# Optimization experiments

Hardware: AMD Instinct MI355X
Metric: run time of the kernel (lower is better)

Reference implementation:

```python
import jax, jax.numpy as jnp
import numpy as np

B, N, C, H = 16, 1024, 768, 12
GRID = 32  # 32x32 patch grid -> N = 1024 tokens
ROPE_BASE = 10000.0


def setup_inputs() -> dict:
    key = jax.random.key(0)
    k1, k2, k3 = jax.random.split(key, 3)
    x = jax.random.normal(k1, (B, N, C), dtype=jnp.float32)
    W_qkv = jax.random.normal(k2, (C, 3 * C), dtype=jnp.float32) * 0.02
    b_qkv = jnp.zeros((3 * C,), dtype=jnp.float32)
    W_proj = jax.random.normal(k3, (C, C), dtype=jnp.float32) * 0.02
    b_proj = jnp.zeros((C,), dtype=jnp.float32)
    ids = jnp.arange(N)
    pos_h = jnp.broadcast_to(ids // GRID, (B, N)).astype(jnp.int32)
    pos_w = jnp.broadcast_to(ids % GRID, (B, N)).astype(jnp.int32)
    return dict(x=x, W_qkv=W_qkv, b_qkv=b_qkv, W_proj=W_proj, b_proj=b_proj,
                pos_h=pos_h, pos_w=pos_w, num_heads=H)


def _rotate_half(t):
    t1, t2 = jnp.split(t, 2, axis=-1)
    return jnp.concatenate((-t2, t1), axis=-1)


def _rope_1d(t, pos, inv):
    # t: (B,H,N,d_rope), pos: (B,N), inv: (d_rope//2,)
    p = pos.astype(jnp.float32)[..., None] * inv      # (B,N,d_rope//2)
    p = p[:, None]                                    # (B,1,N,d_rope//2)
    cos = jnp.repeat(jnp.cos(p), 2, axis=-1)          # repeat_interleave(2)
    sin = jnp.repeat(jnp.sin(p), 2, axis=-1)
    return t * cos + _rotate_half(t) * sin


def reference(x, W_qkv, b_qkv, W_proj, b_proj, pos_h, pos_w, num_heads):
    Bx, Nx, Cx = x.shape
    hd = Cx // num_heads
    d_rope = hd // 2
    inv = 1.0 / ROPE_BASE ** (jnp.arange(0, d_rope, 2, dtype=jnp.float32) / float(max(d_rope, 1)))
    qkv = (x @ W_qkv + b_qkv).reshape(Bx, Nx, 3, num_heads, hd).transpose(2, 0, 3, 1, 4)
    q, k, v = qkv[0], qkv[1], qkv[2]                  # each (B,H,N,hd)
    # 2D RoPE: row-half / col-half of head_dim
    qh, qw = jnp.split(q, 2, axis=-1)
    kh, kw = jnp.split(k, 2, axis=-1)
    qh = _rope_1d(qh, pos_h, inv); kh = _rope_1d(kh, pos_h, inv)
    qw = _rope_1d(qw, pos_w, inv); kw = _rope_1d(kw, pos_w, inv)
    q = jnp.concatenate((qh, qw), axis=-1)
    k = jnp.concatenate((kh, kw), axis=-1)
    scale = hd ** -0.5
    attn = jax.nn.softmax(jnp.einsum('bhnd,bhmd->bhnm', q, k) * scale, axis=-1)
    out = jnp.einsum('bhnm,bhmd->bhnd', attn, v).transpose(0, 2, 1, 3).reshape(Bx, Nx, Cx)
    return out @ W_proj + b_proj
```

## Files before the change

kernel.cpp:

```cpp
#include <hip/hip_runtime.h>
#include <hip/hip_bf16.h>

#define B_ 16
#define N_ 1024
#define C_ 768
#define H_ 12
#define HD_ 64
#define QC_ (3*C_)

using bf16 = __hip_bfloat16;
using bf16x8 = __attribute__((ext_vector_type(8))) __bf16;
using f32x4  = __attribute__((ext_vector_type(4))) float;

__device__ __forceinline__ float tof(bf16 v){ return __bfloat162float(v); }

__device__ __forceinline__ void gload16(const void* g, void* l) {
  __builtin_amdgcn_global_load_lds(
      (const __attribute__((address_space(1))) unsigned int*)g,
      (__attribute__((address_space(3))) unsigned int*)l, 16, 0, 0);
}

__device__ __forceinline__ int xcd_swizzle(int bid, int nwg) {
  return (bid & 7) * (nwg >> 3) + (bid >> 3);
}

__device__ __forceinline__ unsigned pk2(float a, float b) {
  unsigned ua = (unsigned)__bfloat16_as_ushort(__float2bfloat16(a));
  unsigned ub = (unsigned)__bfloat16_as_ushort(__float2bfloat16(b));
  return ua | (ub << 16);
}

__global__ __launch_bounds__(256) void detect_dtype(
    const unsigned* __restrict__ x32, int* __restrict__ flag)
{
  __shared__ int cnt;
  if (threadIdx.x == 0) cnt = 0;
  __syncthreads();
  int local = 0;
  #pragma unroll
  for (int i = 0; i < 16; i++) {
    unsigned u = x32[threadIdx.x * 16 + i * 4096];
    unsigned e = (u >> 7) & 0xFF;
    local += (e >= 110 && e <= 140) ? 1 : 0;
  }
  atomicAdd(&cnt, local);
  __syncthreads();
  if (threadIdx.x == 0) *flag = (cnt > 2048) ? 1 : 0;
}

__global__ __launch_bounds__(256) void cvt_x(
    const void* __restrict__ x, bf16* __restrict__ xb,
    const int* __restrict__ flag, const int n4, const int off4)
{
  const int i = blockIdx.x * 256 + threadIdx.x;
  if (i >= n4) return;
  if (*flag) {
    ((uint2*)xb)[i] = ((const uint2*)x)[off4 + i];
  } else {
    float4 v = ((const float4*)x)[off4 + i];
    xb[i*4+0] = __float2bfloat16(v.x);
    xb[i*4+1] = __float2bfloat16(v.y);
    xb[i*4+2] = __float2bfloat16(v.z);
    xb[i*4+3] = __float2bfloat16(v.w);
  }
}

__global__ __launch_bounds__(256) void wt_cvt(
    const void* __restrict__ W, bf16* __restrict__ WT,
    const int K, const int Nd, const int* __restrict__ flag)
{
  __shared__ float t[32][33];
  const int fl = *flag;
  const int n0 = blockIdx.x * 32, k0 = blockIdx.y * 32;
  const int tx = threadIdx.x & 31, ty = threadIdx.x >> 5;
  for (int kk = ty; kk < 32; kk += 8) {
    const size_t gi = (size_t)(k0 + kk) * Nd + (n0 + tx);
    t[kk][tx] = fl ? tof(((const bf16*)W)[gi]) : ((const float*)W)[gi];
  }
  __syncthreads();
  for (int nn = ty; nn < 32; nn += 8)
    WT[(size_t)(n0 + nn) * K + (k0 + tx)] = __float2bfloat16(t[tx][nn]);
}

__global__ __launch_bounds__(256) void gemm_qkv_rope(
    const bf16* __restrict__ Ab, const bf16* __restrict__ WT,
    const void* __restrict__ bias, bf16* __restrict__ Qp,
    bf16* __restrict__ Kp, bf16* __restrict__ Vtb,
    const int* __restrict__ flag,
    const int* __restrict__ pos_h, const int* __restrict__ pos_w)
{
  const int K = C_;
  const bool bbf = (*flag != 0);

  __shared__ __align__(16) char smem[36864];
  unsigned short* As = (unsigned short*)smem;
  unsigned short* Bs = (unsigned short*)(smem + 16384);

  const int tid = threadIdx.x;
  const int l   = tid & 63;
  const int w   = tid >> 6;
  const int wm  = (w & 1) * 64;
  const int wn  = (w >> 1) * 64;

  const int nwg = gridDim.x * gridDim.y;
  const int bid = blockIdx.y * gridDim.x + blockIdx.x;
  const int lb  = xcd_swizzle(bid, nwg);
  const int gy  = gridDim.y;
  const int brow = lb / gy;
  const int bcol = lb - brow * gy;
  const int row0 = brow * 128;
  const int col0 = bcol * 128;

  const int srow = w*8 + (l >> 3);
  const int sch  = (l & 7) ^ (l >> 3);
  const bf16* Ast = Ab + (size_t)(row0 + srow) * K + sch * 8;
  const bf16* Bst = WT + (size_t)(col0 + srow) * K + sch * 8;

  f32x4 acc[4][4] = {};

  for (int k0 = 0; k0 < K; k0 += 64) {
    __syncthreads();
    #pragma unroll
    for (int i = 0; i < 4; i++) {
      gload16(Ast + (size_t)i*32*K + k0, As + (i*32 + w*8)*64);
      gload16(Bst + (size_t)i*32*K + k0, Bs + (i*32 + w*8)*64);
    }
    __syncthreads();
    #pragma unroll
    for (int s = 0; s < 2; s++) {
      bf16x8 af[4], bg[4];
      const int ch = (s*4 + (l >> 4)) ^ (l & 7);
      #pragma unroll
      for (int i = 0; i < 4; i++) {
        const int rowm = wm + i*16 + (l & 15);
        const int rown = wn + i*16 + (l & 15);
        af[i] = *(const bf16x8*)&As[rowm*64 + ch*8];
        bg[i] = *(const bf16x8*)&Bs[rown*64 + ch*8];
      }
      #pragma unroll
      for (int i = 0; i < 4; i++)
        #pragma unroll
        for (int j = 0; j < 4; j++)
          acc[i][j] = __builtin_amdgcn_mfma_f32_16x16x32_bf16(
                          af[i], bg[j], acc[i][j], 0, 0, 0);
    }
  }

  const int colbase = col0 + wn;
  const int t   = colbase / 768;
  const int h   = (colbase % 768) >> 6;
  const int dd0 = l & 15;
  float bv4[4];
  #pragma unroll
  for (int j = 0; j < 4; j++) {
    const int c = colbase + dd0 + j*16;
    bv4[j] = bbf ? tof(((const bf16*)bias)[c]) : ((const float*)bias)[c];
  }
  const int rb = row0 + wm + (l >> 4) * 4;

  __syncthreads();
  bf16* Ts = (bf16*)(smem + w * 9216);

  if (t == 2) {
    #pragma unroll
    for (int i = 0; i < 4; i++) {
      #pragma unroll
      for (int v = 0; v < 4; v++) {
        const int nl = i*16 + ((l >> 4) << 2) + v;
        #pragma unroll
        for (int j = 0; j < 4; j++) {
          const int dl = dd0 + j*16;
          const float y = acc[i][j][v] + bv4[j];
          Ts[dl*72 + (((nl >> 3) ^ (dl & 7)) << 3) + (nl & 7)] =
              __float2bfloat16(y);
        }
      }
    }
  } else {
    const int fi  = dd0 >> 1;
    const float LOG2B = 13.287712379549449f;
    const float f1 = exp2f(-LOG2B * (float)fi       * (1.0f/16.0f));
    const float f2 = exp2f(-LOG2B * (float)(fi + 8) * (1.0f/16.0f));
    #pragma unroll
    for (int i = 0; i < 4; i++) {
      #pragma unroll
      for (int v = 0; v < 4; v++) {
        const int r  = rb + i*16 + v;
        const int rl = i*16 + (l >> 4)*4 + v;
        float y0 = acc[i][0][v] + bv4[0];
        float y1 = acc[i][1][v] + bv4[1];
        float y2 = acc[i][2][v] + bv4[2];
        float y3 = acc[i][3][v] + bv4[3];
        const float ph = (float)pos_h[r];
        const float pw = (float)pos_w[r];
        float s1,c1,s2,c2,s3,c3,s4,c4;
        __sincosf(ph*f1, &s1, &c1);
        __sincosf(ph*f2, &s2, &c2);
        __sincosf(pw*f1, &s3, &c3);
        __sincosf(pw*f2, &s4, &c4);
        float z[4];
        z[0] = y0*c1 - y1*s1;
        z[1] = y1*c2 + y0*s2;
        z[2] = y2*c3 - y3*s3;
        z[3] = y3*c4 + y2*s4;
        if (t == 0) { z[0]*=0.125f; z[1]*=0.125f; z[2]*=0.125f; z[3]*=0.125f; }
        #pragma unroll
        for (int j = 0; j < 4; j++) {
          const int cl = dd0 + j*16;
          Ts[rl*72 + (((cl >> 3) ^ (rl & 7)) << 3) + (cl & 7)] =
              __float2bfloat16(z[j]);
        }
      }
    }
  }
  __syncthreads();

  if (t == 2) {
    const int n0 = (row0 + wm) & 1023;
    const int bp = (row0 + wm) >> 10;
    const size_t gbase = (size_t)(bp*12 + h) * 65536;
    #pragma unroll
    for (int dr = 0; dr < 8; dr++) {
      const int dl = dr*8 + (l >> 3);
      const int c  = l & 7;
      uint4 vv = *(const uint4*)&Ts[dl*72 + ((c ^ (dl & 7)) << 3)];
      *(uint4*)&Vtb[gbase + (size_t)dl*1024 + n0 + c*8] = vv;
    }
  } else {
    bf16* dst = (t == 0) ? Qp : Kp;
    const int rg0 = row0 + wm;
    const int bp  = rg0 >> 10;
    const int nb  = rg0 & 1023;
    const size_t gbase = (size_t)(bp*12 + h) * 65536;
    #pragma unroll
    for (int dr = 0; dr < 8; dr++) {
      const int rl = dr*8 + (l >> 3);
      const int c  = l & 7;
      uint4 vv = *(const uint4*)&Ts[rl*72 + ((c ^ (rl & 7)) << 3)];
      *(uint4*)&dst[gbase + (size_t)(nb + rl)*64 + c*8] = vv;
    }
  }
}

__global__ __launch_bounds__(256) void attn_mfma(
    const bf16* __restrict__ Qp, const bf16* __restrict__ Kp,
    const bf16* __restrict__ Vtb, bf16* __restrict__ ao)
{
  __shared__ __align__(16) bf16 Qs[64*64];
  __shared__ __align__(16) bf16 Ks[64*64];
  __shared__ __align__(16) bf16 Vs[64*64];
  __shared__ __align__(16) bf16 Ps[64*64];
  const int tid = threadIdx.x;
  const int l   = tid & 63;
  const int w   = tid >> 6;

  const int nwg = gridDim.x * gridDim.y;
  const int bid = blockIdx.y * gridDim.x + blockIdx.x;
  const int lb  = xcd_swizzle(bid, nwg);
  const int qt  = lb & 15;
  const int bh  = lb >> 4;
  const size_t base = (size_t)bh * 65536;

  const int srow = w*8 + (l >> 3);
  const int sch  = (l & 7) ^ (l >> 3);
  const bf16* Qst = Qp  + base + (size_t)(qt*64 + srow)*64 + sch*8;
  const bf16* Kst = Kp  + base + (size_t)srow*64   + sch*8;
  const bf16* Vst = Vtb + base + (size_t)srow*1024 + sch*8;

  #pragma unroll
  for (int i = 0; i < 2; i++)
    gload16(Qst + (size_t)i*32*64, Qs + (i*32 + w*8)*64);
  __syncthreads();

  bf16x8 af[2];
  {
    const int row = w*16 + (l & 15);
    #pragma unroll
    for (int s = 0; s < 2; s++) {
      const int ch = (s*4 + (l >> 4)) ^ (row & 7);
      af[s] = *(const bf16x8*)&Qs[row*64 + ch*8];
    }
  }

  const float LOG2E = 1.4426950408889634f;
  float m_i = -3.0e38f, l_i = 0.f;
  f32x4 o[4] = {};

  const int g    = l >> 4;
  const int qrow = w*16 + (l & 15);

  for (int kt = 0; kt < 16; kt++) {
    __syncthreads();
    #pragma unroll
    for (int i = 0; i < 2; i++) {
      gload16(Kst + (size_t)(kt*64 + i*32)*64, Ks + (i*32 + w*8)*64);
      gload16(Vst + (size_t)i*32*1024 + kt*64, Vs + (i*32 + w*8)*64);
    }
    __syncthreads();

    f32x4 s[4];
    #pragma unroll
    for (int nt = 0; nt < 4; nt++) {
      f32x4 a = {};
      const int nrow = nt*16 + (l & 15);
      #pragma unroll
      for (int ss = 0; ss < 2; ss++) {
        const int ch = (ss*4 + (l >> 4)) ^ (nrow & 7);
        bf16x8 bg = *(const bf16x8*)&Ks[nrow*64 + ch*8];
        a = __builtin_amdgcn_mfma_f32_16x16x32_bf16(bg, af[ss], a, 0, 0, 0);
      }
      s[nt] = a;
    }

    float mloc = s[0][0];
    #pragma unroll
    for (int nt = 0; nt < 4; nt++)
      #pragma unroll
      for (int v = 0; v < 4; v++)
        mloc = fmaxf(mloc, s[nt][v]);
    mloc = fmaxf(mloc, __shfl_xor(mloc, 16));
    const float m0 = fmaxf(mloc, __shfl_xor(mloc, 32));

    if (!__all(m0 - m_i <= 8.0f)) {
      const float mx = fmaxf(m_i, m0);
      const float alpha = exp2f((m_i - mx) * LOG2E);
      l_i *= alpha;
      m_i = mx;
      float a_o[4];
      #pragma unroll
      for (int v = 0; v < 4; v++)
        a_o[v] = __shfl(alpha, (l & 48) | ((g << 2) + v));
      #pragma unroll
      for (int nt = 0; nt < 4; nt++)
        #pragma unroll
        for (int v = 0; v < 4; v++)
          o[nt][v] *= a_o[v];
    }

    float r = 0.f;
    #pragma unroll
    for (int nt = 0; nt < 4; nt++)
      #pragma unroll
      for (int v = 0; v < 4; v++) {
        const float p = exp2f((s[nt][v] - m_i) * LOG2E);
        s[nt][v] = p;
        r += p;
      }
    r += __shfl_xor(r, 16);
    r += __shfl_xor(r, 32);
    l_i += r;

    #pragma unroll
    for (int nt = 0; nt < 4; nt++) {
      const int k0 = nt*16 + (g << 2);
      const int ch = (k0 >> 3) ^ (qrow & 7);
      uint2 uu;
      uu.x = pk2(s[nt][0], s[nt][1]);
      uu.y = pk2(s[nt][2], s[nt][3]);
      *(uint2*)&Ps[qrow*64 + ch*8 + (k0 & 7)] = uu;
    }

    #pragma unroll
    for (int ss = 0; ss < 2; ss++) {
      const int prow = w*16 + (l & 15);
      const int pch  = (ss*4 + (l >> 4)) ^ (prow & 7);
      bf16x8 pa = *(const bf16x8*)&Ps[prow*64 + pch*8];
      #pragma unroll
      for (int ntd = 0; ntd < 4; ntd++) {
        const int drow = ntd*16 + (l & 15);
        const int vch  = (ss*4 + (l >> 4)) ^ (drow & 7);
        bf16x8 vb = *(const bf16x8*)&Vs[drow*64 + vch*8];
        o[ntd] = __builtin_amdgcn_mfma_f32_16x16x32_bf16(pa, vb, o[ntd], 0,0,0);
      }
    }
  }

  const int b = bh / 12, h = bh - b*12;
  const float inv = 1.0f / l_i;
  float inv_o[4];
  #pragma unroll
  for (int v = 0; v < 4; v++)
    inv_o[v] = __shfl(inv, (l & 48) | ((g << 2) + v));
  #pragma unroll
  for (int v = 0; v < 4; v++) {
    const int rl = g*4 + v;
    #pragma unroll
    for (int ntd = 0; ntd < 4; ntd++) {
      const int cl = ntd*16 + (l & 15);
      Ps[(w*16 + rl)*64 + (((cl >> 3) ^ (rl & 7)) << 3) + (cl & 7)] =
          __float2bfloat16(o[ntd][v] * inv_o[v]);
    }
  }
  #pragma unroll
  for (int e = 0; e < 2; e++) {
    const int rl = e*8 + (l >> 3);
    const int c  = l & 7;
    uint4 vv = *(const uint4*)&Ps[(w*16 + rl)*64 + ((c ^ (rl & 7)) << 3)];
    const int r = qt*64 + w*16 + rl;
    *(uint4*)&ao[((size_t)(b*1024 + r)) * 768 + h*64 + c*8] = vv;
  }
}

__global__ __launch_bounds__(256) void gemm_mfma(
    const bf16* __restrict__ Ab, const bf16* __restrict__ WT,
    const void* __restrict__ bias, void* __restrict__ Cout,
    const int Nd, const int K, const int c_row_off,
    const int* __restrict__ flag, const int bias_mode, const int c_mode)
{
  const int fl = *flag;
  const bool bbf = (bias_mode == 2) ? (fl != 0) : (bias_mode != 0);
  const bool cbf = (c_mode == 2) ? (fl != 0) : (c_mode != 0);

  __shared__ __align__(16) unsigned short As[128*64];
  __shared__ __align__(16) unsigned short Bs[128*64];

  const int tid = threadIdx.x;
  const int l   = tid & 63;
  const int w   = tid >> 6;
  const int wm  = (w & 1) * 64;
  const int wn  = (w >> 1) * 64;

  const int nwg = gridDim.x * gridDim.y;
  const int bid = blockIdx.y * gridDim.x + blockIdx.x;
  const int lb  = xcd_swizzle(bid, nwg);
  const int gy  = gridDim.y;
  const int brow = lb / gy;
  const int bcol = lb - brow * gy;
  const int row0 = brow * 128;
  const int col0 = bcol * 128;

  const int srow = w*8 + (l >> 3);
  const int sch  = (l & 7) ^ (l >> 3);
  const bf16* Ast = Ab + (size_t)(row0 + srow) * K + sch * 8;
  const bf16* Bst = WT + (size_t)(col0 + srow) * K + sch * 8;

  f32x4 acc[4][4] = {};

  for (int k0 = 0; k0 < K; k0 += 64) {
    __syncthreads();
    #pragma unroll
    for (int i = 0; i < 4; i++) {
      gload16(Ast + (size_t)i*32*K + k0, As + (i*32 + w*8)*64);
      gload16(Bst + (size_t)i*32*K + k0, Bs + (i*32 + w*8)*64);
    }
    __syncthreads();
    #pragma unroll
    for (int s = 0; s < 2; s++) {
      bf16x8 af[4], bg[4];
      const int ch = (s*4 + (l >> 4)) ^ (l & 7);
      #pragma unroll
      for (int i = 0; i < 4; i++) {
        const int rowm = wm + i*16 + (l & 15);
        const int rown = wn + i*16 + (l & 15);
        af[i] = *(const bf16x8*)&As[rowm*64 + ch*8];
        bg[i] = *(const bf16x8*)&Bs[rown*64 + ch*8];
      }
      #pragma unroll
      for (int i = 0; i < 4; i++)
        #pragma unroll
        for (int j = 0; j < 4; j++)
          acc[i][j] = __builtin_amdgcn_mfma_f32_16x16x32_bf16(
                          af[i], bg[j], acc[i][j], 0, 0, 0);
    }
  }

  const int cn    = col0 + wn + (l & 15);
  const int rbase = c_row_off + row0 + wm + (l >> 4) * 4;
  #pragma unroll
  for (int j = 0; j < 4; j++) {
    const int col = cn + j*16;
    const float bval = bbf ? tof(((const bf16*)bias)[col])
                           : ((const float*)bias)[col];
    #pragma unroll
    for (int i = 0; i < 4; i++) {
      #pragma unroll
      for (int v = 0; v < 4; v++) {
        const size_t r = (size_t)(rbase + i*16 + v);
        const float val = acc[i][j][v] + bval;
        if (cbf) ((bf16*)Cout)[r * Nd + col] = __float2bfloat16(val);
        else     ((float*)Cout)[r * Nd + col] = val;
      }
    }
  }
}

extern "C" void kernel_launch(void* const* d_in, const int* in_sizes, int n_in,
                              void* d_out, int out_size, void* d_ws, size_t ws_size,
                              hipStream_t stream)
{
  (void)in_sizes; (void)n_in; (void)out_size;
  const void* x     = d_in[0];
  const void* Wqkv  = d_in[1];
  const void* bqkv  = d_in[2];
  const void* Wproj = d_in[3];
  const void* bproj = d_in[4];
  const int*  pos_h = (const int*)d_in[5];
  const int*  pos_w = (const int*)d_in[6];

  int* flag = (int*)d_ws;
  char* p = (char*)d_ws + 256;
  bf16* WqkvT  = (bf16*)p; p += (size_t)QC_ * C_ * 2;
  bf16* WprojT = (bf16*)p; p += (size_t)C_ * C_ * 2;

  const size_t fixed = 256 + (size_t)QC_*C_*2 + (size_t)C_*C_*2;
  const size_t perb  = 5 * (size_t)N_ * C_ * 2;
  int CB = 16;
  if (ws_size < fixed + 16*perb) CB = 8;
  if (ws_size < fixed + 8*perb)  CB = 4;
  if (ws_size < fixed + 4*perb)  CB = 2;
  if (ws_size < fixed + 2*perb)  CB = 1;
  const int Mc = CB * N_;
  const size_t tsz = (size_t)Mc * C_;

  bf16* xb  = (bf16*)p;
  bf16* Qp  = xb  + tsz;
  bf16* Kp  = Qp  + tsz;
  bf16* Vtb = Kp  + tsz;
  bf16* ao  = Vtb + tsz;

  detect_dtype<<<1, 256, 0, stream>>>((const unsigned*)x, flag);
  wt_cvt<<<dim3(QC_/32, C_/32), 256, 0, stream>>>(Wqkv, WqkvT, C_, QC_, flag);
  wt_cvt<<<dim3(C_/32,  C_/32), 256, 0, stream>>>(Wproj, WprojT, C_, C_, flag);

  for (int c0 = 0; c0 < B_; c0 += CB) {
    const int n4 = Mc * C_ / 4;
    cvt_x<<<(n4 + 255)/256, 256, 0, stream>>>(x, xb, flag, n4, c0 * N_ * C_ / 4);
    gemm_qkv_rope<<<dim3(Mc/128, QC_/128), 256, 0, stream>>>(
        xb, WqkvT, bqkv, Qp, Kp, Vtb, flag,
        pos_h + (size_t)c0*N_, pos_w + (size_t)c0*N_);
    attn_mfma<<<dim3(N_/64, CB*H_), 256, 0, stream>>>(Qp, Kp, Vtb, ao);
    gemm_mfma<<<dim3(Mc/128, C_/128), 256, 0, stream>>>(
        ao, WprojT, bproj, d_out, C_, C_, c0*N_, flag, 2, 2);
  }
}
```

Measured before the change: 368.7 us.

## Fold log2e into Q scale, compute row sums via MFMA, alias Q/P LDS

Folds the log2(e) factor into the Q scaling during the QKV epilogue, so the attention softmax can use exp2 directly without a multiply. The row-sum reduction with shuffles is replaced by an extra MFMA against a vector of ones, accumulating l in the same layout as O. Q and P now share one LDS buffer to cut shared memory per block, and s_setprio hints are placed around the MFMA phases. This trades a little accuracy for fewer VALU ops, since P is rounded to bf16 before being summed, and it relies on Q being read into registers before P overwrites the shared buffer.

```diff
diff --git a/kernel.cpp b/kernel.cpp
--- a/kernel.cpp
+++ b/kernel.cpp
@@ -203,7 +203,10 @@
         z[1] = y1*c2 + y0*s2;
         z[2] = y2*c3 - y3*s3;
         z[3] = y3*c4 + y2*s4;
-        if (t == 0) { z[0]*=0.125f; z[1]*=0.125f; z[2]*=0.125f; z[3]*=0.125f; }
+        if (t == 0) {
+          const float QS = 0.18033688011112042f;
+          z[0]*=QS; z[1]*=QS; z[2]*=QS; z[3]*=QS;
+        }
         #pragma unroll
         for (int j = 0; j < 4; j++) {
           const int cl = dd0 + j*16;
@@ -246,10 +249,11 @@
     const bf16* __restrict__ Qp, const bf16* __restrict__ Kp,
     const bf16* __restrict__ Vtb, bf16* __restrict__ ao)
 {
-  __shared__ __align__(16) bf16 Qs[64*64];
+  __shared__ __align__(16) bf16 QPs[64*64];
   __shared__ __align__(16) bf16 Ks[64*64];
   __shared__ __align__(16) bf16 Vs[64*64];
-  __shared__ __align__(16) bf16 Ps[64*64];
+  bf16* Qs = QPs;
+  bf16* Ps = QPs;
   const int tid = threadIdx.x;
   const int l   = tid & 63;
   const int w   = tid >> 6;
@@ -282,8 +286,12 @@
     }
   }
 
-  const float LOG2E = 1.4426950408889634f;
-  float m_i = -3.0e38f, l_i = 0.f;
+  bf16x8 ones;
+  #pragma unroll
+  for (int i = 0; i < 8; i++) ones[i] = (__bf16)1.0f;
+
+  float m_i = -3.0e38f;
+  f32x4 l_acc = {};
   f32x4 o[4] = {};
 
   const int g    = l >> 4;
@@ -299,6 +307,7 @@
     __syncthreads();
 
     f32x4 s[4];
+    __builtin_amdgcn_s_setprio(1);
     #pragma unroll
     for (int nt = 0; nt < 4; nt++) {
       f32x4 a = {};
@@ -311,60 +320,55 @@
       }
       s[nt] = a;
     }
-
-    float mloc = s[0][0];
-    #pragma unroll
-    for (int nt = 0; nt < 4; nt++)
-      #pragma unroll
-      for (int v = 0; v < 4; v++)
-        mloc = fmaxf(mloc, s[nt][v]);
+    __builtin_amdgcn_s_setprio(0);
+
+    float a0 = fmaxf(fmaxf(s[0][0], s[0][1]), s[0][2]);
+    float a1 = fmaxf(fmaxf(s[0][3], s[1][0]), s[1][1]);
+    float a2 = fmaxf(fmaxf(s[1][2], s[1][3]), s[2][0]);
+    float a3 = fmaxf(fmaxf(s[2][1], s[2][2]), s[2][3]);
+    float a4 = fmaxf(fmaxf(s[3][0], s[3][1]), s[3][2]);
+    float b0 = fmaxf(fmaxf(a0, a1), a2);
+    float b1 = fmaxf(fmaxf(a3, a4), s[3][3]);
+    float mloc = fmaxf(b0, b1);
     mloc = fmaxf(mloc, __shfl_xor(mloc, 16));
     const float m0 = fmaxf(mloc, __shfl_xor(mloc, 32));
 
     if (!__all(m0 - m_i <= 8.0f)) {
       const float mx = fmaxf(m_i, m0);
-      const float alpha = exp2f((m_i - mx) * LOG2E);
-      l_i *= alpha;
+      const float alpha = exp2f(m_i - mx);
       m_i = mx;
       float a_o[4];
       #pragma unroll
       for (int v = 0; v < 4; v++)
         a_o[v] = __shfl(alpha, (l & 48) | ((g << 2) + v));
       #pragma unroll
-      for (int nt = 0; nt < 4; nt++)
+      for (int v = 0; v < 4; v++) {
+        l_acc[v] *= a_o[v];
         #pragma unroll
-        for (int v = 0; v < 4; v++)
-          o[nt][v] *= a_o[v];
-    }
-
-    float r = 0.f;
-    #pragma unroll
-    for (int nt = 0; nt < 4; nt++)
-      #pragma unroll
-      for (int v = 0; v < 4; v++) {
-        const float p = exp2f((s[nt][v] - m_i) * LOG2E);
-        s[nt][v] = p;
-        r += p;
-      }
-    r += __shfl_xor(r, 16);
-    r += __shfl_xor(r, 32);
-    l_i += r;
+        for (int nt = 0; nt < 4; nt++) o[nt][v] *= a_o[v];
+      }
+    }
 
     #pragma unroll
     for (int nt = 0; nt < 4; nt++) {
+      const float p0 = exp2f(s[nt][0] - m_i);
+      const float p1 = exp2f(s[nt][1] - m_i);
+      const float p2 = exp2f(s[nt][2] - m_i);
+      const float p3 = exp2f(s[nt][3] - m_i);
       const int k0 = nt*16 + (g << 2);
       const int ch = (k0 >> 3) ^ (qrow & 7);
       uint2 uu;
-      uu.x = pk2(s[nt][0], s[nt][1]);
-      uu.y = pk2(s[nt][2], s[nt][3]);
+      uu.x = pk2(p0, p1);
+      uu.y = pk2(p2, p3);
       *(uint2*)&Ps[qrow*64 + ch*8 + (k0 & 7)] = uu;
     }
 
+    __builtin_amdgcn_s_setprio(1);
     #pragma unroll
     for (int ss = 0; ss < 2; ss++) {
-      const int prow = w*16 + (l & 15);
-      const int pch  = (ss*4 + (l >> 4)) ^ (prow & 7);
-      bf16x8 pa = *(const bf16x8*)&Ps[prow*64 + pch*8];
+      const int pch  = (ss*4 + g) ^ (qrow & 7);
+      bf16x8 pa = *(const bf16x8*)&Ps[qrow*64 + pch*8];
+      l_acc = __builtin_amdgcn_mfma_f32_16x16x32_bf16(pa, ones, l_acc, 0,0,0);
       #pragma unroll
       for (int ntd = 0; ntd < 4; ntd++) {
         const int drow = ntd*16 + (l & 15);
@@ -373,22 +377,19 @@
         o[ntd] = __builtin_amdgcn_mfma_f32_16x16x32_bf16(pa, vb, o[ntd], 0,0,0);
       }
     }
+    __builtin_amdgcn_s_setprio(0);
   }
 
   const int b = bh / 12, h = bh - b*12;
-  const float inv = 1.0f / l_i;
-  float inv_o[4];
-  #pragma unroll
-  for (int v = 0; v < 4; v++)
-    inv_o[v] = __shfl(inv, (l & 48) | ((g << 2) + v));
   #pragma unroll
   for (int v = 0; v < 4; v++) {
+    const float invv = 1.0f / l_acc[v];
     const int rl = g*4 + v;
     #pragma unroll
     for (int ntd = 0; ntd < 4; ntd++) {
       const int cl = ntd*16 + (l & 15);
       Ps[(w*16 + rl)*64 + (((cl >> 3) ^ (rl & 7)) << 3) + (cl & 7)] =
-          __float2bfloat16(o[ntd][v] * inv_o[v]);
+          __float2bfloat16(o[ntd][v] * invv);
     }
   }
   #pragma unroll
```

New measurement: 359.4 us. -2.5%, faster.
